# Kernel tuning notes

Measured on AMD Instinct MI355X. Metric: run time of the kernel, lower is better.

Reference implementation:

```python
import jax, jax.numpy as jnp
import numpy as np

B, S, D, L = 128, 256, 256, 3          # graphs, nodes/graph (=max_set_size), feat dim, gnn layers
E = 524288                              # edges per graph-set (avg degree 16)
N = B * S                               # total nodes per side
TAU, N_SINK, EPS_GIN, BN_EPS = 0.1, 20, 1.0, 1e-5


def setup_inputs() -> dict:
    key = jax.random.key(0)
    ks = jax.random.split(key, 16)
    sc = 1.0 / np.sqrt(D)
    inp = {
        "features_1": jax.random.normal(ks[0], (N, D), jnp.float32),
        "features_2": jax.random.normal(ks[1], (N, D), jnp.float32),
        "edge_index_1": jax.random.randint(ks[2], (2, E), 0, N),
        "edge_index_2": jax.random.randint(ks[3], (2, E), 0, N),
        "u_noise": jax.random.uniform(ks[4], (B, S, S), jnp.float32),
        # stacked GIN MLP params (3 identical-shape layers)
        "gin_w1": jax.random.normal(ks[5], (L, D, D), jnp.float32) * sc,
        "gin_b1": jnp.zeros((L, D), jnp.float32),
        "gin_w2": jax.random.normal(ks[6], (L, D, D), jnp.float32) * sc,
        "gin_b2": jnp.zeros((L, D), jnp.float32),
        "gin_gamma": jnp.ones((L, D), jnp.float32),
        "gin_beta": jnp.zeros((L, D), jnp.float32),
        # fc_transform1/2 and bilinear W
        "fc1_w": jax.random.normal(ks[7], (D, D), jnp.float32) * sc,
        "fc1_b": jnp.zeros((D,), jnp.float32),
        "fc2_w": jax.random.normal(ks[8], (D, D), jnp.float32) * sc,
        "fc2_b": jnp.zeros((D,), jnp.float32),
        "W": jax.random.normal(ks[9], (D, D), jnp.float32) * sc,
    }
    return inp


def _forward(features_1, features_2, u_noise, gin_w1, gin_b1, gin_w2, gin_b2,
             gin_gamma, gin_beta, fc1_w, fc1_b, fc2_w, fc2_b, W,
             edge_index_1, edge_index_2):
    def gin_stack(x, ei):
        src, dst = ei[0], ei[1]
        for l in range(L):
            # GINConv: nn((1+eps)*x + sum_{j->i} x_j), eps=True -> 1.0
            aggr = jax.ops.segment_sum(x[src], dst, num_segments=N)
            h = (1.0 + EPS_GIN) * x + aggr
            h = jax.nn.relu(h @ gin_w1[l] + gin_b1[l])
            h = h @ gin_w2[l] + gin_b2[l]
            mu = jnp.mean(h, axis=0)
            var = jnp.var(h, axis=0)                      # BatchNorm1d, training stats
            h = gin_gamma[l] * (h - mu) * jax.lax.rsqrt(var + BN_EPS) + gin_beta[l]
            x = jax.nn.relu(h)                            # outer relu (dropout p=0)
        return x

    g1 = gin_stack(features_1, edge_index_1).reshape(B, S, D)  # all graphs have S nodes -> no pad
    g2 = gin_stack(features_2, edge_index_2).reshape(B, S, D)

    def transform(g):
        return jax.nn.relu(g @ fc1_w + fc1_b) @ fc2_w + fc2_b

    m1 = transform(g1)   # masks are all-ones since every graph is full-size
    m2 = transform(g2)
    scores = jnp.einsum('bsd,de,bte->bst', m1, W, m2)          # [B,S,S]

    gumbel = -jnp.log(-jnp.log(u_noise + 1e-20) + 1e-20)
    log_alpha = (scores + gumbel) / TAU
    for _ in range(N_SINK):
        log_alpha = log_alpha - jax.scipy.special.logsumexp(log_alpha, axis=-1, keepdims=True)
        log_alpha = log_alpha - jax.scipy.special.logsumexp(log_alpha, axis=-2, keepdims=True)
    P = jnp.exp(log_alpha)

    p = jnp.sum(g1 - jnp.matmul(P, g2), axis=(1, 2))           # [B]
    p = (p - p.min()) / (p.max() - p.min())
    return jnp.exp(-p)


def reference(features_1, features_2, edge_index_1, edge_index_2, u_noise,
              gin_w1, gin_b1, gin_w2, gin_b2, gin_gamma, gin_beta,
              fc1_w, fc1_b, fc2_w, fc2_b, W):
    return _forward(features_1, features_2, u_noise, gin_w1, gin_b1, gin_w2, gin_b2,
                    gin_gamma, gin_beta, fc1_w, fc1_b, fc2_w, fc2_b, W,
                    edge_index_1, edge_index_2)
```

## Files before the change

kernel.cpp:

```cpp
#include <hip/hip_runtime.h>


constexpr int NNODE = 32768;
constexpr int NEDGE = 524288;

typedef __attribute__((ext_vector_type(8))) short bf16x8;
typedef __attribute__((ext_vector_type(4))) float f32x4;

__device__ __forceinline__ float bf2f(unsigned short u) {
  return __uint_as_float((unsigned)u << 16);
}
__device__ __forceinline__ unsigned short f2bf(float f) {
  unsigned u = __float_as_uint(f);
  return (unsigned short)((u + 0x7FFFu + ((u >> 16) & 1u)) >> 16);
}
__device__ __forceinline__ unsigned packbf(float a, float b) {
  return (unsigned)f2bf(a) | ((unsigned)f2bf(b) << 16);
}

__global__ __launch_bounds__(256) void k_conv(const float* __restrict__ a,
                                              const float* __restrict__ b,
                                              unsigned short* __restrict__ out) {
  size_t i = (size_t)blockIdx.x * 256 + threadIdx.x;
  const float* src = (i < 2097152) ? (a + i * 4) : (b + (i - 2097152) * 4);
  float4 v = *(const float4*)src;
  ushort4 o;
  o.x = f2bf(v.x); o.y = f2bf(v.y); o.z = f2bf(v.z); o.w = f2bf(v.w);
  *(ushort4*)(out + i * 4) = o;
}

__global__ __launch_bounds__(256) void k_wprep(const float* __restrict__ gw1,
                                               const float* __restrict__ gw2,
                                               unsigned short* __restrict__ Wt) {
  __shared__ float sh[64][65];
  int b = blockIdx.x;
  int mat = b >> 4, tile = b & 15;
  int tr = (tile >> 2) * 64, tc = (tile & 3) * 64;
  const float* src = (mat < 3) ? (gw1 + (size_t)mat * 65536) : (gw2 + (size_t)(mat - 3) * 65536);
  int t = threadIdx.x;
#pragma unroll
  for (int i = 0; i < 4; i++) {
    int c = t + i * 256;
    int row = c >> 4, c4 = (c & 15) * 4;
    float4 v = *(const float4*)(src + (size_t)(tr + row) * 256 + tc + c4);
    sh[row][c4] = v.x; sh[row][c4 + 1] = v.y; sh[row][c4 + 2] = v.z; sh[row][c4 + 3] = v.w;
  }
  __syncthreads();
#pragma unroll
  for (int i = 0; i < 2; i++) {
    int c = t + i * 256;
    int n = c >> 3, kc = (c & 7) * 8;
    unsigned short e[8];
#pragma unroll
    for (int j = 0; j < 8; j++) e[j] = f2bf(sh[kc + j][n]);
    uint4 o;
    o.x = e[0] | ((unsigned)e[1] << 16);
    o.y = e[2] | ((unsigned)e[3] << 16);
    o.z = e[4] | ((unsigned)e[5] << 16);
    o.w = e[6] | ((unsigned)e[7] << 16);
    *(uint4*)(Wt + (size_t)mat * 65536 + (size_t)(tc + n) * 256 + tr + kc) = o;
  }
}

__global__ void k_degree2(const int* __restrict__ e1, const int* __restrict__ e2,
                          int* __restrict__ cnt) {
  int b = blockIdx.x;
  int side = b >> 11;
  int e = (b & 2047) * 256 + threadIdx.x;
  const int* dst = (side ? e2 : e1) + NEDGE;
  atomicAdd(&cnt[side * NNODE + dst[e]], 1);
}

__global__ void k_scan2(const int* __restrict__ cnt, int* __restrict__ off,
                        int* __restrict__ cur) {
  __shared__ int sh[1024];
  int side = blockIdx.x;
  const int* c = cnt + side * NNODE;
  int* of = off + side * (NNODE + 64);
  int* cu = cur + side * NNODE;
  int t = threadIdx.x;
  int base = t * 32;
  int loc[32];
  int s = 0;
#pragma unroll
  for (int j = 0; j < 32; j++) { loc[j] = c[base + j]; s += loc[j]; }
  sh[t] = s;
  __syncthreads();
  for (int d = 1; d < 1024; d <<= 1) {
    int v = (t >= d) ? sh[t - d] : 0;
    __syncthreads();
    sh[t] += v;
    __syncthreads();
  }
  int run = sh[t] - s;
#pragma unroll
  for (int j = 0; j < 32; j++) { of[base + j] = run; cu[base + j] = run; run += loc[j]; }
  if (t == 1023) of[NNODE] = run;
}

__global__ void k_scatter2(const int* __restrict__ e1, const int* __restrict__ e2,
                           int* __restrict__ cur, int* __restrict__ srcs) {
  int b = blockIdx.x;
  int side = b >> 11;
  int e = (b & 2047) * 256 + threadIdx.x;
  const int* ei = (side ? e2 : e1);
  int d = ei[NEDGE + e];
  int p = atomicAdd(&cur[side * NNODE + d], 1);
  srcs[side * NEDGE + p] = ei[e];
}

template <bool BN>
__global__ __launch_bounds__(512, 4) void k_layer(
    const unsigned short* __restrict__ x,
    const int* __restrict__ off, const int* __restrict__ srcs,
    const float* __restrict__ pstats,
    const float* __restrict__ pgamma, const float* __restrict__ pbeta,
    const unsigned short* __restrict__ w1t,
    const unsigned short* __restrict__ w2t,
    const float* __restrict__ b1, const float* __restrict__ b2,
    float* __restrict__ stats,
    unsigned short* __restrict__ hout) {
  __shared__ __align__(16) char smem[69632];
  char* sA = smem;
  char* sA2 = smem;
  char* sW = smem + 32768;
  float2* red = (float2*)(smem + 65536);
  int tid = threadIdx.x;
  int lane = tid & 63, wid = tid >> 6;
  int wm = wid & 1, wn = wid >> 1;
  int q = lane >> 4, r = lane & 15;
  const int sw = (r & 7) << 4;
  int b = blockIdx.x;
  int side = b >> 9;
  size_t grow0 = (size_t)side * NNODE + (size_t)(b & 511) * 64;

  {
    int hw = tid >> 5, sub = tid & 31;
    float sc[8], shf[8];
    if (BN) {
      int c0 = sub * 8;
      const float* cs = pstats + side * 512;
      const float invn = 1.f / 32768.f;
#pragma unroll
      for (int j = 0; j < 8; j++) {
        float mu = cs[c0 + j] * invn;
        float var = cs[256 + c0 + j] * invn - mu * mu;
        float s = pgamma[c0 + j] * rsqrtf(var + 1e-5f);
        sc[j] = s; shf[j] = pbeta[c0 + j] - mu * s;
      }
    }
    const uint4* X = (const uint4*)x;
    size_t rbase = (size_t)side * NNODE;
    const int* offs = off + side * (NNODE + 64);
    const int* sr = srcs + (size_t)side * NEDGE;
#pragma unroll 1
    for (int nn = 0; nn < 4; nn++) {
      int lrow = hw * 4 + nn;
      int n = (int)(b & 511) * 64 + lrow;
      float a[8];
#pragma unroll
      for (int j = 0; j < 8; j++) a[j] = 0.f;
      auto acc8 = [&](uint4 u, float w) {
        unsigned uu[4] = {u.x, u.y, u.z, u.w};
#pragma unroll
        for (int j = 0; j < 4; j++) {
          float lo = __uint_as_float(uu[j] << 16);
          float hi = __uint_as_float(uu[j] & 0xFFFF0000u);
          if (BN) {
            lo = fmaxf(fmaf(lo, sc[2 * j], shf[2 * j]), 0.f);
            hi = fmaxf(fmaf(hi, sc[2 * j + 1], shf[2 * j + 1]), 0.f);
          }
          a[2 * j] = fmaf(lo, w, a[2 * j]);
          a[2 * j + 1] = fmaf(hi, w, a[2 * j + 1]);
        }
      };
      acc8(X[(rbase + n) * 32 + sub], 2.f);
      int e = offs[n], ee = offs[n + 1];
      for (; e + 3 < ee; e += 4) {
        int i0 = sr[e], i1 = sr[e + 1], i2 = sr[e + 2], i3 = sr[e + 3];
        uint4 u0 = X[(rbase + i0) * 32 + sub];
        uint4 u1 = X[(rbase + i1) * 32 + sub];
        uint4 u2 = X[(rbase + i2) * 32 + sub];
        uint4 u3 = X[(rbase + i3) * 32 + sub];
        acc8(u0, 1.f); acc8(u1, 1.f); acc8(u2, 1.f); acc8(u3, 1.f);
      }
      for (; e < ee; e++) acc8(X[(rbase + sr[e]) * 32 + sub], 1.f);
      uint4 o;
      o.x = packbf(a[0], a[1]); o.y = packbf(a[2], a[3]);
      o.z = packbf(a[4], a[5]); o.w = packbf(a[6], a[7]);
      *(uint4*)(sA + lrow * 512 + ((sub * 16) ^ ((lrow & 7) << 4))) = o;
    }
  }

  auto stageW = [&](const unsigned short* wsrc, int k0) {
    for (int c = tid; c < 2048; c += 512) {
      int row = c >> 3, cb = (c & 7) * 16;
      float4 v = *(const float4*)(wsrc + (size_t)row * 256 + k0 + (c & 7) * 8);
      *(float4*)(sW + row * 128 + (cb ^ ((row & 7) << 4))) = v;
    }
  };

  f32x4 acc[2][4];
#pragma unroll
  for (int mi = 0; mi < 2; mi++)
#pragma unroll
    for (int ni = 0; ni < 4; ni++) acc[mi][ni] = (f32x4){0.f, 0.f, 0.f, 0.f};

  stageW(w1t, 0);
  __syncthreads();

  for (int k0 = 0; k0 < 256; k0 += 64) {
#pragma unroll
    for (int ks = 0; ks < 2; ks++) {
      bf16x8 af[2], bfr[4];
      int cbA = (k0 * 2 + ks * 64 + q * 16) ^ sw;
      int cbW = (ks * 64 + q * 16) ^ sw;
#pragma unroll
      for (int mi = 0; mi < 2; mi++)
        af[mi] = *(const bf16x8*)(sA + (wm * 32 + mi * 16 + r) * 512 + cbA);
#pragma unroll
      for (int ni = 0; ni < 4; ni++)
        bfr[ni] = *(const bf16x8*)(sW + (wn * 64 + ni * 16 + r) * 128 + cbW);
#pragma unroll
      for (int mi = 0; mi < 2; mi++)
#pragma unroll
        for (int ni = 0; ni < 4; ni++)
          acc[mi][ni] = __builtin_amdgcn_mfma_f32_16x16x32_bf16(af[mi], bfr[ni], acc[mi][ni], 0, 0, 0);
    }
    __syncthreads();
    if (k0 < 192) {
      stageW(w1t, k0 + 64);
      __syncthreads();
    }
  }

  float b1v[4];
#pragma unroll
  for (int ni = 0; ni < 4; ni++) b1v[ni] = b1[wn * 64 + ni * 16 + r];
#pragma unroll
  for (int mi = 0; mi < 2; mi++)
#pragma unroll
    for (int ni = 0; ni < 4; ni++)
#pragma unroll
      for (int j = 0; j < 4; j++) {
        float o = fmaxf(acc[mi][ni][j] + b1v[ni], 0.f);
        int rowc = wm * 32 + mi * 16 + q * 4 + j;
        int colc = wn * 64 + ni * 16 + r;
        *(unsigned short*)(sA2 + rowc * 512 + ((colc * 2) ^ (((q * 4 + j) & 7) << 4))) = f2bf(o);
      }
#pragma unroll
  for (int mi = 0; mi < 2; mi++)
#pragma unroll
    for (int ni = 0; ni < 4; ni++) acc[mi][ni] = (f32x4){0.f, 0.f, 0.f, 0.f};
  stageW(w2t, 0);
  __syncthreads();

  for (int k0 = 0; k0 < 256; k0 += 64) {
#pragma unroll
    for (int ks = 0; ks < 2; ks++) {
      bf16x8 af[2], bfr[4];
      int cbA = (k0 * 2 + ks * 64 + q * 16) ^ sw;
      int cbW = (ks * 64 + q * 16) ^ sw;
#pragma unroll
      for (int mi = 0; mi < 2; mi++)
        af[mi] = *(const bf16x8*)(sA2 + (wm * 32 + mi * 16 + r) * 512 + cbA);
#pragma unroll
      for (int ni = 0; ni < 4; ni++)
        bfr[ni] = *(const bf16x8*)(sW + (wn * 64 + ni * 16 + r) * 128 + cbW);
#pragma unroll
      for (int mi = 0; mi < 2; mi++)
#pragma unroll
        for (int ni = 0; ni < 4; ni++)
          acc[mi][ni] = __builtin_amdgcn_mfma_f32_16x16x32_bf16(af[mi], bfr[ni], acc[mi][ni], 0, 0, 0);
    }
    __syncthreads();
    if (k0 < 192) {
      stageW(w2t, k0 + 64);
      __syncthreads();
    }
  }

  float b2v[4];
#pragma unroll
  for (int ni = 0; ni < 4; ni++) b2v[ni] = b2[wn * 64 + ni * 16 + r];
#pragma unroll
  for (int ni = 0; ni < 4; ni++) {
    float ss = 0.f, sq = 0.f;
#pragma unroll
    for (int mi = 0; mi < 2; mi++)
#pragma unroll
      for (int j = 0; j < 4; j++) {
        float o = acc[mi][ni][j] + b2v[ni];
        acc[mi][ni][j] = o;
        ss += o; sq += o * o;
      }
    ss += __shfl_xor(ss, 16, 64); ss += __shfl_xor(ss, 32, 64);
    sq += __shfl_xor(sq, 16, 64); sq += __shfl_xor(sq, 32, 64);
    if (q == 0) {
      float2 w; w.x = ss; w.y = sq;
      red[(wn * 64 + ni * 16 + r) * 2 + wm] = w;
    }
  }
#pragma unroll
  for (int mi = 0; mi < 2; mi++)
#pragma unroll
    for (int ni = 0; ni < 4; ni++)
#pragma unroll
      for (int j = 0; j < 4; j++) {
        int rowc = wm * 32 + mi * 16 + q * 4 + j;
        int colc = wn * 64 + ni * 16 + r;
        *(unsigned short*)(sW + rowc * 512 + ((colc * 2) ^ (((q * 4 + j) & 7) << 4))) =
            f2bf(acc[mi][ni][j]);
      }
  __syncthreads();
  float* cs = stats + side * 512;
  if (tid < 256) {
    float2 a = red[tid * 2], c2 = red[tid * 2 + 1];
    atomicAdd(&cs[tid], a.x + c2.x);
    atomicAdd(&cs[256 + tid], a.y + c2.y);
  }
  for (int c = tid; c < 2048; c += 512) {
    int row = c >> 5, cb = (c & 31) * 16;
    float4 v = *(const float4*)(sW + row * 512 + (cb ^ ((row & 7) << 4)));
    *(float4*)(hout + (grow0 + row) * 256 + (c & 31) * 8) = v;
  }
}

__global__ __launch_bounds__(256) void k_gsum(
    const unsigned short* __restrict__ h, const float* __restrict__ stats,
    const float* __restrict__ gamma, const float* __restrict__ beta,
    float* __restrict__ sg) {
  int b = blockIdx.x;
  int side = b >> 7, g = b & 127;
  int t = threadIdx.x;
  int c0 = (t & 63) * 4, rg = t >> 6;
  const float* cs = stats + side * 512;
  float sc[4], sh_[4];
#pragma unroll
  for (int j = 0; j < 4; j++) {
    float mu = cs[c0 + j] * (1.f / 32768.f);
    float var = cs[256 + c0 + j] * (1.f / 32768.f) - mu * mu;
    float s = gamma[c0 + j] * rsqrtf(var + 1e-5f);
    sc[j] = s; sh_[j] = beta[c0 + j] - mu * s;
  }
  size_t base = (size_t)side * NNODE + (size_t)g * 256;
  float acc = 0.f;
  for (int k = 0; k < 64; k++) {
    int row = rg + k * 4;
    ushort4 u = *(const ushort4*)(h + (base + row) * 256 + c0);
    acc += fmaxf(fmaf(bf2f(u.x), sc[0], sh_[0]), 0.f);
    acc += fmaxf(fmaf(bf2f(u.y), sc[1], sh_[1]), 0.f);
    acc += fmaxf(fmaf(bf2f(u.z), sc[2], sh_[2]), 0.f);
    acc += fmaxf(fmaf(bf2f(u.w), sc[3], sh_[3]), 0.f);
  }
  __shared__ float red[256];
  red[t] = acc;
  __syncthreads();
  if (t < 64) {
    float s = red[t] + red[t + 64] + red[t + 128] + red[t + 192];
#pragma unroll
    for (int m = 1; m < 64; m <<= 1) s += __shfl_xor(s, m, 64);
    if (t == 0) sg[b] = s;
  }
}

__global__ void k_final(const float* __restrict__ sg1, const float* __restrict__ sg2,
                        float* __restrict__ out) {
  int t = threadIdx.x;
  float a = sg1[t] - sg2[t];
  float b = sg1[t + 64] - sg2[t + 64];
  float mn = fminf(a, b), mx = fmaxf(a, b);
#pragma unroll
  for (int msk = 1; msk < 64; msk <<= 1) {
    mn = fminf(mn, __shfl_xor(mn, msk, 64));
    mx = fmaxf(mx, __shfl_xor(mx, msk, 64));
  }
  float inv = 1.0f / (mx - mn);
  out[t] = __expf(-(a - mn) * inv);
  out[t + 64] = __expf(-(b - mn) * inv);
}

extern "C" void kernel_launch(void* const* d_in, const int* in_sizes, int n_in,
                              void* d_out, int out_size, void* d_ws, size_t ws_size,
                              hipStream_t stream) {
  (void)in_sizes; (void)n_in; (void)out_size; (void)ws_size;
  const float* f1 = (const float*)d_in[0];
  const float* f2 = (const float*)d_in[1];
  const int* e1 = (const int*)d_in[2];
  const int* e2 = (const int*)d_in[3];
  const float* gw1 = (const float*)d_in[5];
  const float* gb1 = (const float*)d_in[6];
  const float* gw2 = (const float*)d_in[7];
  const float* gb2 = (const float*)d_in[8];
  const float* gga = (const float*)d_in[9];
  const float* gbe = (const float*)d_in[10];
  float* out = (float*)d_out;

  char* ws = (char*)d_ws;
  size_t o = 0;
  auto alloc = [&](size_t bytes) { void* p = ws + o; o += (bytes + 255) & ~(size_t)255; return p; };
  unsigned short* hb0 = (unsigned short*)alloc(2ull * NNODE * 256 * 2);
  unsigned short* hb1 = (unsigned short*)alloc(2ull * NNODE * 256 * 2);
  unsigned short* Wt = (unsigned short*)alloc(6ull * 65536 * 2);
  float* stats = (float*)alloc(3 * 1024 * 4);
  float* sg = (float*)alloc(256 * 4);
  int* cnt = (int*)alloc(2 * NNODE * 4);
  int* off = (int*)alloc(2 * (NNODE + 64) * 4);
  int* cur = (int*)alloc(2 * NNODE * 4);
  int* srcs = (int*)alloc(2ull * NEDGE * 4);

  (void)hipMemsetAsync(stats, 0, 3 * 1024 * 4, stream);
  (void)hipMemsetAsync(cnt, 0, 2 * NNODE * 4, stream);

  k_conv<<<16384, 256, 0, stream>>>(f1, f2, hb0);
  k_wprep<<<96, 256, 0, stream>>>(gw1, gw2, Wt);
  k_degree2<<<4096, 256, 0, stream>>>(e1, e2, cnt);
  k_scan2<<<2, 1024, 0, stream>>>(cnt, off, cur);
  k_scatter2<<<4096, 256, 0, stream>>>(e1, e2, cur, srcs);

  unsigned short* hb[2] = {hb0, hb1};
  for (int l = 0; l < 3; l++) {
    unsigned short* xin = hb[l & 1];
    unsigned short* hout = hb[1 - (l & 1)];
    if (l == 0)
      k_layer<false><<<1024, 512, 0, stream>>>(
          xin, off, srcs, nullptr, nullptr, nullptr,
          Wt + (size_t)l * 65536, Wt + (size_t)(3 + l) * 65536,
          gb1 + l * 256, gb2 + l * 256, stats + l * 1024, hout);
    else
      k_layer<true><<<1024, 512, 0, stream>>>(
          xin, off, srcs, stats + (l - 1) * 1024, gga + (l - 1) * 256, gbe + (l - 1) * 256,
          Wt + (size_t)l * 65536, Wt + (size_t)(3 + l) * 65536,
          gb1 + l * 256, gb2 + l * 256, stats + l * 1024, hout);
  }

  k_gsum<<<256, 256, 0, stream>>>(hb1, stats + 2 * 1024, gga + 512, gbe + 512, sg);
  k_final<<<1, 64, 0, stream>>>(sg, sg + 128, out);
}
```

Measured before the change: 501.4 us.

## Bucket CSR edges by source range to improve gather locality across blocks

Edges are split into four source-node buckets (by src>>13) within each destination's CSR segment, using per-bucket counts, offsets and cursors. The aggregation loop now walks bucket by bucket across a warp's four rows, so concurrent gathers across the GPU hit a narrower slice of the feature table at a time, which is meant to improve L2/cache hit rates. The W1 staging into shared memory is also moved ahead of aggregation so its global loads overlap with the gather. In exchange it adds an extra preprocessing kernel, larger count arrays, and keeps 32 accumulators per thread, which raises register pressure.

```diff
diff --git a/kernel.cpp b/kernel.cpp
--- a/kernel.cpp
+++ b/kernel.cpp
@@ -62,28 +62,31 @@
   }
 }
 
-__global__ void k_degree2(const int* __restrict__ e1, const int* __restrict__ e2,
-                          int* __restrict__ cnt) {
+__global__ void k_degree4(const int* __restrict__ e1, const int* __restrict__ e2,
+                          int* __restrict__ cnt4) {
   int b = blockIdx.x;
   int side = b >> 11;
   int e = (b & 2047) * 256 + threadIdx.x;
-  const int* dst = (side ? e2 : e1) + NEDGE;
-  atomicAdd(&cnt[side * NNODE + dst[e]], 1);
-}
-
-__global__ void k_scan2(const int* __restrict__ cnt, int* __restrict__ off,
-                        int* __restrict__ cur) {
+  const int* ei = (side ? e2 : e1);
+  int s = ei[e], d = ei[NEDGE + e];
+  atomicAdd(&cnt4[((size_t)side * NNODE + d) * 4 + (s >> 13)], 1);
+}
+
+__global__ void k_scan2(const int* __restrict__ cnt4, int* __restrict__ off) {
   __shared__ int sh[1024];
   int side = blockIdx.x;
-  const int* c = cnt + side * NNODE;
+  const int* c4 = cnt4 + (size_t)side * NNODE * 4;
   int* of = off + side * (NNODE + 64);
-  int* cu = cur + side * NNODE;
   int t = threadIdx.x;
   int base = t * 32;
   int loc[32];
   int s = 0;
 #pragma unroll
-  for (int j = 0; j < 32; j++) { loc[j] = c[base + j]; s += loc[j]; }
+  for (int j = 0; j < 32; j++) {
+    int n4 = (base + j) * 4;
+    loc[j] = c4[n4] + c4[n4 + 1] + c4[n4 + 2] + c4[n4 + 3];
+    s += loc[j];
+  }
   sh[t] = s;
   __syncthreads();
   for (int d = 1; d < 1024; d <<= 1) {
@@ -94,25 +97,41 @@
   }
   int run = sh[t] - s;
 #pragma unroll
-  for (int j = 0; j < 32; j++) { of[base + j] = run; cu[base + j] = run; run += loc[j]; }
+  for (int j = 0; j < 32; j++) { of[base + j] = run; run += loc[j]; }
   if (t == 1023) of[NNODE] = run;
 }
 
-__global__ void k_scatter2(const int* __restrict__ e1, const int* __restrict__ e2,
-                           int* __restrict__ cur, int* __restrict__ srcs) {
+__global__ __launch_bounds__(256) void k_suboff(const int* __restrict__ cnt4,
+                                                const int* __restrict__ off,
+                                                int* __restrict__ off2,
+                                                int* __restrict__ cur2) {
+  int i = blockIdx.x * 256 + threadIdx.x;
+  int side = i >> 15, n = i & 32767;
+  int base = off[side * (NNODE + 64) + n];
+  size_t i4 = (size_t)i * 4;
+  int c0 = cnt4[i4], c1 = cnt4[i4 + 1], c2 = cnt4[i4 + 2];
+  int o0 = base, o1 = base + c0, o2 = o1 + c1, o3 = o2 + c2;
+  off2[i4] = o0; off2[i4 + 1] = o1; off2[i4 + 2] = o2; off2[i4 + 3] = o3;
+  cur2[i4] = o0; cur2[i4 + 1] = o1; cur2[i4 + 2] = o2; cur2[i4 + 3] = o3;
+}
+
+__global__ void k_scatter4(const int* __restrict__ e1, const int* __restrict__ e2,
+                           int* __restrict__ cur2, int* __restrict__ srcs) {
   int b = blockIdx.x;
   int side = b >> 11;
   int e = (b & 2047) * 256 + threadIdx.x;
   const int* ei = (side ? e2 : e1);
-  int d = ei[NEDGE + e];
-  int p = atomicAdd(&cur[side * NNODE + d], 1);
-  srcs[side * NEDGE + p] = ei[e];
+  int s = ei[e], d = ei[NEDGE + e];
+  int p = atomicAdd(&cur2[((size_t)side * NNODE + d) * 4 + (s >> 13)], 1);
+  srcs[(size_t)side * NEDGE + p] = s;
 }
 
 template <bool BN>
 __global__ __launch_bounds__(512, 4) void k_layer(
     const unsigned short* __restrict__ x,
-    const int* __restrict__ off, const int* __restrict__ srcs,
+    const int* __restrict__ off,
+    const int* __restrict__ off2,
+    const int* __restrict__ srcs,
     const float* __restrict__ pstats,
     const float* __restrict__ pgamma, const float* __restrict__ pbeta,
     const unsigned short* __restrict__ w1t,
@@ -134,6 +153,16 @@
   int side = b >> 9;
   size_t grow0 = (size_t)side * NNODE + (size_t)(b & 511) * 64;
 
+  auto stageW = [&](const unsigned short* wsrc, int k0) {
+    for (int c = tid; c < 2048; c += 512) {
+      int row = c >> 3, cb = (c & 7) * 16;
+      float4 v = *(const float4*)(wsrc + (size_t)row * 256 + k0 + (c & 7) * 8);
+      *(float4*)(sW + row * 128 + (cb ^ ((row & 7) << 4))) = v;
+    }
+  };
+
+  stageW(w1t, 0);
+
   {
     int hw = tid >> 5, sub = tid & 31;
     float sc[8], shf[8];
@@ -152,61 +181,71 @@
     const uint4* X = (const uint4*)x;
     size_t rbase = (size_t)side * NNODE;
     const int* offs = off + side * (NNODE + 64);
+    const int* offs2 = off2 + (size_t)side * NNODE * 4;
     const int* sr = srcs + (size_t)side * NEDGE;
+    int nbase = (int)(b & 511) * 64 + hw * 4;
+
+    float a[4][8];
+#pragma unroll
+    for (int nn = 0; nn < 4; nn++)
+#pragma unroll
+      for (int j = 0; j < 8; j++) a[nn][j] = 0.f;
+
+    auto acc8 = [&](float* ap, uint4 u, float w) {
+      unsigned uu[4] = {u.x, u.y, u.z, u.w};
+#pragma unroll
+      for (int j = 0; j < 4; j++) {
+        float lo = __uint_as_float(uu[j] << 16);
+        float hi = __uint_as_float(uu[j] & 0xFFFF0000u);
+        if (BN) {
+          lo = fmaxf(fmaf(lo, sc[2 * j], shf[2 * j]), 0.f);
+          hi = fmaxf(fmaf(hi, sc[2 * j + 1], shf[2 * j + 1]), 0.f);
+        }
+        ap[2 * j] = fmaf(lo, w, ap[2 * j]);
+        ap[2 * j + 1] = fmaf(hi, w, ap[2 * j + 1]);
+      }
+    };
+
+#pragma unroll
+    for (int nn = 0; nn < 4; nn++)
+      acc8(a[nn], X[(rbase + nbase + nn) * 32 + sub], 2.f);
+
 #pragma unroll 1
+    for (int c = 0; c < 4; c++) {
+#pragma unroll
+      for (int nn = 0; nn < 4; nn++) {
+        int n = nbase + nn;
+        int e = offs2[(n << 2) + c];
+        int ee = (c < 3) ? offs2[(n << 2) + c + 1] : offs[n + 1];
+        for (; e + 3 < ee; e += 4) {
+          int i0 = sr[e], i1 = sr[e + 1], i2 = sr[e + 2], i3 = sr[e + 3];
+          uint4 u0 = X[(rbase + i0) * 32 + sub];
+          uint4 u1 = X[(rbase + i1) * 32 + sub];
+          uint4 u2 = X[(rbase + i2) * 32 + sub];
+          uint4 u3 = X[(rbase + i3) * 32 + sub];
+          acc8(a[nn], u0, 1.f); acc8(a[nn], u1, 1.f);
+          acc8(a[nn], u2, 1.f); acc8(a[nn], u3, 1.f);
+        }
+        for (; e < ee; e++) acc8(a[nn], X[(rbase + sr[e]) * 32 + sub], 1.f);
+      }
+    }
+
+#pragma unroll
     for (int nn = 0; nn < 4; nn++) {
       int lrow = hw * 4 + nn;
-      int n = (int)(b & 511) * 64 + lrow;
-      float a[8];
-#pragma unroll
-      for (int j = 0; j < 8; j++) a[j] = 0.f;
-      auto acc8 = [&](uint4 u, float w) {
-        unsigned uu[4] = {u.x, u.y, u.z, u.w};
-#pragma unroll
-        for (int j = 0; j < 4; j++) {
-          float lo = __uint_as_float(uu[j] << 16);
-          float hi = __uint_as_float(uu[j] & 0xFFFF0000u);
-          if (BN) {
-            lo = fmaxf(fmaf(lo, sc[2 * j], shf[2 * j]), 0.f);
-            hi = fmaxf(fmaf(hi, sc[2 * j + 1], shf[2 * j + 1]), 0.f);
-          }
-          a[2 * j] = fmaf(lo, w, a[2 * j]);
-          a[2 * j + 1] = fmaf(hi, w, a[2 * j + 1]);
-        }
-      };
-      acc8(X[(rbase + n) * 32 + sub], 2.f);
-      int e = offs[n], ee = offs[n + 1];
-      for (; e + 3 < ee; e += 4) {
-        int i0 = sr[e], i1 = sr[e + 1], i2 = sr[e + 2], i3 = sr[e + 3];
-        uint4 u0 = X[(rbase + i0) * 32 + sub];
-        uint4 u1 = X[(rbase + i1) * 32 + sub];
-        uint4 u2 = X[(rbase + i2) * 32 + sub];
-        uint4 u3 = X[(rbase + i3) * 32 + sub];
-        acc8(u0, 1.f); acc8(u1, 1.f); acc8(u2, 1.f); acc8(u3, 1.f);
-      }
-      for (; e < ee; e++) acc8(X[(rbase + sr[e]) * 32 + sub], 1.f);
       uint4 o;
-      o.x = packbf(a[0], a[1]); o.y = packbf(a[2], a[3]);
-      o.z = packbf(a[4], a[5]); o.w = packbf(a[6], a[7]);
+      o.x = packbf(a[nn][0], a[nn][1]); o.y = packbf(a[nn][2], a[nn][3]);
+      o.z = packbf(a[nn][4], a[nn][5]); o.w = packbf(a[nn][6], a[nn][7]);
       *(uint4*)(sA + lrow * 512 + ((sub * 16) ^ ((lrow & 7) << 4))) = o;
     }
   }
 
-  auto stageW = [&](const unsigned short* wsrc, int k0) {
-    for (int c = tid; c < 2048; c += 512) {
-      int row = c >> 3, cb = (c & 7) * 16;
-      float4 v = *(const float4*)(wsrc + (size_t)row * 256 + k0 + (c & 7) * 8);
-      *(float4*)(sW + row * 128 + (cb ^ ((row & 7) << 4))) = v;
-    }
-  };
-
   f32x4 acc[2][4];
 #pragma unroll
   for (int mi = 0; mi < 2; mi++)
 #pragma unroll
     for (int ni = 0; ni < 4; ni++) acc[mi][ni] = (f32x4){0.f, 0.f, 0.f, 0.f};
 
-  stageW(w1t, 0);
   __syncthreads();
 
   for (int k0 = 0; k0 < 256; k0 += 64) {
@@ -404,19 +443,21 @@
   unsigned short* Wt = (unsigned short*)alloc(6ull * 65536 * 2);
   float* stats = (float*)alloc(3 * 1024 * 4);
   float* sg = (float*)alloc(256 * 4);
-  int* cnt = (int*)alloc(2 * NNODE * 4);
+  int* cnt4 = (int*)alloc(2ull * NNODE * 4 * 4);
   int* off = (int*)alloc(2 * (NNODE + 64) * 4);
-  int* cur = (int*)alloc(2 * NNODE * 4);
+  int* off2 = (int*)alloc(2ull * NNODE * 4 * 4);
+  int* cur2 = (int*)alloc(2ull * NNODE * 4 * 4);
   int* srcs = (int*)alloc(2ull * NEDGE * 4);
 
   (void)hipMemsetAsync(stats, 0, 3 * 1024 * 4, stream);
-  (void)hipMemsetAsync(cnt, 0, 2 * NNODE * 4, stream);
+  (void)hipMemsetAsync(cnt4, 0, 2ull * NNODE * 4 * 4, stream);
 
   k_conv<<<16384, 256, 0, stream>>>(f1, f2, hb0);
   k_wprep<<<96, 256, 0, stream>>>(gw1, gw2, Wt);
-  k_degree2<<<4096, 256, 0, stream>>>(e1, e2, cnt);
-  k_scan2<<<2, 1024, 0, stream>>>(cnt, off, cur);
-  k_scatter2<<<4096, 256, 0, stream>>>(e1, e2, cur, srcs);
+  k_degree4<<<4096, 256, 0, stream>>>(e1, e2, cnt4);
+  k_scan2<<<2, 1024, 0, stream>>>(cnt4, off);
+  k_suboff<<<256, 256, 0, stream>>>(cnt4, off, off2, cur2);
+  k_scatter4<<<4096, 256, 0, stream>>>(e1, e2, cur2, srcs);
 
   unsigned short* hb[2] = {hb0, hb1};
   for (int l = 0; l < 3; l++) {
@@ -424,12 +465,12 @@
     unsigned short* hout = hb[1 - (l & 1)];
     if (l == 0)
       k_layer<false><<<1024, 512, 0, stream>>>(
-          xin, off, srcs, nullptr, nullptr, nullptr,
+          xin, off, off2, srcs, nullptr, nullptr, nullptr,
           Wt + (size_t)l * 65536, Wt + (size_t)(3 + l) * 65536,
           gb1 + l * 256, gb2 + l * 256, stats + l * 1024, hout);
     else
       k_layer<true><<<1024, 512, 0, stream>>>(
-          xin, off, srcs, stats + (l - 1) * 1024, gga + (l - 1) * 256, gbe + (l - 1) * 256,
+          xin, off, off2, srcs, stats + (l - 1) * 1024, gga + (l - 1) * 256, gbe + (l - 1) * 256,
           Wt + (size_t)l * 65536, Wt + (size_t)(3 + l) * 65536,
           gb1 + l * 256, gb2 + l * 256, stats + l * 1024, hout);
   }
```

Measured after the change: 572.1 us. 14.1% more time.

## Enlarge GIN layer row tile to 128 and fuse prep kernels

Applied to the files above, without the earlier changes.

The fused gather+MLP layer kernel now handles 128 rows per block instead of 64. Each warp computes a 64x64 output tile, and weights are staged in 32-wide K slices stored in a k-blocked layout with a new swizzle. This halves the number of blocks and the total weight re-staging per row. Separately, the conversion, weight-transpose and degree-count kernels are merged into one launch, and the prefix scan uses wave shuffles instead of a shared-memory Hillis-Steele loop. The larger LDS footprint (80KB) cuts resident blocks per CU, which may hurt latency hiding in the gather phase.

```diff
diff --git a/kernel.cpp b/kernel.cpp
--- a/kernel.cpp
+++ b/kernel.cpp
@@ -18,81 +18,94 @@
   return (unsigned)f2bf(a) | ((unsigned)f2bf(b) << 16);
 }
 
-__global__ __launch_bounds__(256) void k_conv(const float* __restrict__ a,
-                                              const float* __restrict__ b,
-                                              unsigned short* __restrict__ out) {
-  size_t i = (size_t)blockIdx.x * 256 + threadIdx.x;
-  const float* src = (i < 2097152) ? (a + i * 4) : (b + (i - 2097152) * 4);
-  float4 v = *(const float4*)src;
-  ushort4 o;
-  o.x = f2bf(v.x); o.y = f2bf(v.y); o.z = f2bf(v.z); o.w = f2bf(v.w);
-  *(ushort4*)(out + i * 4) = o;
-}
-
-__global__ __launch_bounds__(256) void k_wprep(const float* __restrict__ gw1,
-                                               const float* __restrict__ gw2,
-                                               unsigned short* __restrict__ Wt) {
+__global__ __launch_bounds__(256) void k_prep(
+    const float* __restrict__ f1, const float* __restrict__ f2,
+    unsigned short* __restrict__ hb0,
+    const float* __restrict__ gw1, const float* __restrict__ gw2,
+    unsigned short* __restrict__ Wt,
+    const int* __restrict__ e1, const int* __restrict__ e2,
+    int* __restrict__ cnt) {
   __shared__ float sh[64][65];
-  int b = blockIdx.x;
-  int mat = b >> 4, tile = b & 15;
-  int tr = (tile >> 2) * 64, tc = (tile & 3) * 64;
-  const float* src = (mat < 3) ? (gw1 + (size_t)mat * 65536) : (gw2 + (size_t)(mat - 3) * 65536);
-  int t = threadIdx.x;
-#pragma unroll
-  for (int i = 0; i < 4; i++) {
-    int c = t + i * 256;
-    int row = c >> 4, c4 = (c & 15) * 4;
-    float4 v = *(const float4*)(src + (size_t)(tr + row) * 256 + tc + c4);
-    sh[row][c4] = v.x; sh[row][c4 + 1] = v.y; sh[row][c4 + 2] = v.z; sh[row][c4 + 3] = v.w;
-  }
-  __syncthreads();
-#pragma unroll
-  for (int i = 0; i < 2; i++) {
-    int c = t + i * 256;
-    int n = c >> 3, kc = (c & 7) * 8;
-    unsigned short e[8];
-#pragma unroll
-    for (int j = 0; j < 8; j++) e[j] = f2bf(sh[kc + j][n]);
-    uint4 o;
-    o.x = e[0] | ((unsigned)e[1] << 16);
-    o.y = e[2] | ((unsigned)e[3] << 16);
-    o.z = e[4] | ((unsigned)e[5] << 16);
-    o.w = e[6] | ((unsigned)e[7] << 16);
-    *(uint4*)(Wt + (size_t)mat * 65536 + (size_t)(tc + n) * 256 + tr + kc) = o;
-  }
-}
-
-__global__ void k_degree2(const int* __restrict__ e1, const int* __restrict__ e2,
-                          int* __restrict__ cnt) {
-  int b = blockIdx.x;
-  int side = b >> 11;
-  int e = (b & 2047) * 256 + threadIdx.x;
-  const int* dst = (side ? e2 : e1) + NEDGE;
-  atomicAdd(&cnt[side * NNODE + dst[e]], 1);
-}
-
-__global__ void k_scan2(const int* __restrict__ cnt, int* __restrict__ off,
-                        int* __restrict__ cur) {
-  __shared__ int sh[1024];
+  int b = blockIdx.x, t = threadIdx.x;
+  if (b < 16384) {
+    size_t i = (size_t)b * 256 + t;
+    const float* src = (i < 2097152) ? (f1 + i * 4) : (f2 + (i - 2097152) * 4);
+    float4 v = *(const float4*)src;
+    ushort4 o;
+    o.x = f2bf(v.x); o.y = f2bf(v.y); o.z = f2bf(v.z); o.w = f2bf(v.w);
+    *(ushort4*)(hb0 + i * 4) = o;
+  } else if (b < 16480) {
+    int bb = b - 16384;
+    int mat = bb >> 4, tile = bb & 15;
+    int tr = (tile >> 2) * 64, tc = (tile & 3) * 64;
+    const float* src = (mat < 3) ? (gw1 + (size_t)mat * 65536) : (gw2 + (size_t)(mat - 3) * 65536);
+#pragma unroll
+    for (int i = 0; i < 4; i++) {
+      int c = t + i * 256;
+      int row = c >> 4, c4 = (c & 15) * 4;
+      float4 v = *(const float4*)(src + (size_t)(tr + row) * 256 + tc + c4);
+      sh[row][c4] = v.x; sh[row][c4 + 1] = v.y; sh[row][c4 + 2] = v.z; sh[row][c4 + 3] = v.w;
+    }
+    __syncthreads();
+#pragma unroll
+    for (int i = 0; i < 2; i++) {
+      int c = t + i * 256;
+      int n = c >> 3, kc = (c & 7) * 8;
+      unsigned short e[8];
+#pragma unroll
+      for (int j = 0; j < 8; j++) e[j] = f2bf(sh[kc + j][n]);
+      uint4 o;
+      o.x = e[0] | ((unsigned)e[1] << 16);
+      o.y = e[2] | ((unsigned)e[3] << 16);
+      o.z = e[4] | ((unsigned)e[5] << 16);
+      o.w = e[6] | ((unsigned)e[7] << 16);
+      int kg = tr + kc;
+      size_t idx = (size_t)mat * 65536 + (size_t)(kg >> 5) * 8192 + (size_t)(tc + n) * 32 + (kg & 31);
+      *(uint4*)(Wt + idx) = o;
+    }
+  } else {
+    int bb = b - 16480;
+    int side = bb >> 11;
+    int e = (bb & 2047) * 256 + t;
+    const int* dst = (side ? e2 : e1) + NEDGE;
+    atomicAdd(&cnt[side * NNODE + dst[e]], 1);
+  }
+}
+
+__global__ __launch_bounds__(1024) void k_scan2(const int* __restrict__ cnt,
+                                                int* __restrict__ off,
+                                                int* __restrict__ cur) {
   int side = blockIdx.x;
   const int* c = cnt + side * NNODE;
   int* of = off + side * (NNODE + 64);
   int* cu = cur + side * NNODE;
   int t = threadIdx.x;
+  int lane = t & 63, wv = t >> 6;
   int base = t * 32;
   int loc[32];
   int s = 0;
 #pragma unroll
   for (int j = 0; j < 32; j++) { loc[j] = c[base + j]; s += loc[j]; }
-  sh[t] = s;
-  __syncthreads();
-  for (int d = 1; d < 1024; d <<= 1) {
-    int v = (t >= d) ? sh[t - d] : 0;
-    __syncthreads();
-    sh[t] += v;
-    __syncthreads();
-  }
-  int run = sh[t] - s;
+  int tot = s;
+#pragma unroll
+  for (int d = 1; d < 64; d <<= 1) {
+    int v = __shfl_up(s, d, 64);
+    if (lane >= d) s += v;
+  }
+  __shared__ int ws[16];
+  if (lane == 63) ws[wv] = s;
+  __syncthreads();
+  if (t < 16) {
+    int w = ws[t];
+#pragma unroll
+    for (int d = 1; d < 16; d <<= 1) {
+      int v = __shfl_up(w, d, 64);
+      if (t >= d) w += v;
+    }
+    ws[t] = w;
+  }
+  __syncthreads();
+  int run = s - tot + (wv ? ws[wv - 1] : 0);
 #pragma unroll
   for (int j = 0; j < 32; j++) { of[base + j] = run; cu[base + j] = run; run += loc[j]; }
   if (t == 1023) of[NNODE] = run;
@@ -120,19 +133,33 @@
     const float* __restrict__ b1, const float* __restrict__ b2,
     float* __restrict__ stats,
     unsigned short* __restrict__ hout) {
-  __shared__ __align__(16) char smem[69632];
+  __shared__ __align__(16) char smem[81920];
   char* sA = smem;
   char* sA2 = smem;
-  char* sW = smem + 32768;
+  char* sW = smem + 65536;
   float2* red = (float2*)(smem + 65536);
   int tid = threadIdx.x;
   int lane = tid & 63, wid = tid >> 6;
   int wm = wid & 1, wn = wid >> 1;
   int q = lane >> 4, r = lane & 15;
-  const int sw = (r & 7) << 4;
+  const int swA = (r & 7) << 4;
+  const int swW = ((r >> 1) & 3) << 4;
   int b = blockIdx.x;
-  int side = b >> 9;
-  size_t grow0 = (size_t)side * NNODE + (size_t)(b & 511) * 64;
+  int side = b >> 8;
+  size_t grow0 = (size_t)side * NNODE + (size_t)(b & 255) * 128;
+
+  auto stageW = [&](const unsigned short* wsrc, int k0) {
+    const unsigned short* basep = wsrc + (size_t)(k0 >> 5) * 8192;
+#pragma unroll
+    for (int it = 0; it < 2; it++) {
+      int c = tid + it * 512;
+      int row = c >> 2, ch = c & 3;
+      float4 v = *(const float4*)(basep + (size_t)c * 8);
+      *(float4*)(sW + row * 64 + ((ch * 16) ^ (((row >> 1) & 3) << 4))) = v;
+    }
+  };
+
+  stageW(w1t, 0);
 
   {
     int hw = tid >> 5, sub = tid & 31;
@@ -153,10 +180,12 @@
     size_t rbase = (size_t)side * NNODE;
     const int* offs = off + side * (NNODE + 64);
     const int* sr = srcs + (size_t)side * NEDGE;
+    int nbase = (int)(b & 255) * 128;
+
 #pragma unroll 1
-    for (int nn = 0; nn < 4; nn++) {
-      int lrow = hw * 4 + nn;
-      int n = (int)(b & 511) * 64 + lrow;
+    for (int nn = 0; nn < 8; nn++) {
+      int lrow = hw * 8 + nn;
+      int n = nbase + lrow;
       float a[8];
 #pragma unroll
       for (int j = 0; j < 8; j++) a[j] = 0.f;
@@ -192,44 +221,32 @@
     }
   }
 
-  auto stageW = [&](const unsigned short* wsrc, int k0) {
-    for (int c = tid; c < 2048; c += 512) {
-      int row = c >> 3, cb = (c & 7) * 16;
-      float4 v = *(const float4*)(wsrc + (size_t)row * 256 + k0 + (c & 7) * 8);
-      *(float4*)(sW + row * 128 + (cb ^ ((row & 7) << 4))) = v;
-    }
-  };
-
-  f32x4 acc[2][4];
-#pragma unroll
-  for (int mi = 0; mi < 2; mi++)
+  f32x4 acc[4][4];
+#pragma unroll
+  for (int mi = 0; mi < 4; mi++)
 #pragma unroll
     for (int ni = 0; ni < 4; ni++) acc[mi][ni] = (f32x4){0.f, 0.f, 0.f, 0.f};
 
-  stageW(w1t, 0);
-  __syncthreads();
-
-  for (int k0 = 0; k0 < 256; k0 += 64) {
-#pragma unroll
-    for (int ks = 0; ks < 2; ks++) {
-      bf16x8 af[2], bfr[4];
-      int cbA = (k0 * 2 + ks * 64 + q * 16) ^ sw;
-      int cbW = (ks * 64 + q * 16) ^ sw;
-#pragma unroll
-      for (int mi = 0; mi < 2; mi++)
-        af[mi] = *(const bf16x8*)(sA + (wm * 32 + mi * 16 + r) * 512 + cbA);
+  __syncthreads();
+
+  for (int k0 = 0; k0 < 256; k0 += 32) {
+    bf16x8 af[4], bfr[4];
+    int cbA = (k0 * 2 + q * 16) ^ swA;
+    int cbW = (q * 16) ^ swW;
+#pragma unroll
+    for (int mi = 0; mi < 4; mi++)
+      af[mi] = *(const bf16x8*)(sA + (wm * 64 + mi * 16 + r) * 512 + cbA);
+#pragma unroll
+    for (int ni = 0; ni < 4; ni++)
+      bfr[ni] = *(const bf16x8*)(sW + (wn * 64 + ni * 16 + r) * 64 + cbW);
+#pragma unroll
+    for (int mi = 0; mi < 4; mi++)
 #pragma unroll
       for (int ni = 0; ni < 4; ni++)
-        bfr[ni] = *(const bf16x8*)(sW + (wn * 64 + ni * 16 + r) * 128 + cbW);
-#pragma unroll
-      for (int mi = 0; mi < 2; mi++)
-#pragma unroll
-        for (int ni = 0; ni < 4; ni++)
-          acc[mi][ni] = __builtin_amdgcn_mfma_f32_16x16x32_bf16(af[mi], bfr[ni], acc[mi][ni], 0, 0, 0);
-    }
+        acc[mi][ni] = __builtin_amdgcn_mfma_f32_16x16x32_bf16(af[mi], bfr[ni], acc[mi][ni], 0, 0, 0);
     __syncthreads();
-    if (k0 < 192) {
-      stageW(w1t, k0 + 64);
+    if (k0 < 224) {
+      stageW(w1t, k0 + 32);
       __syncthreads();
     }
   }
@@ -238,44 +255,41 @@
 #pragma unroll
   for (int ni = 0; ni < 4; ni++) b1v[ni] = b1[wn * 64 + ni * 16 + r];
 #pragma unroll
-  for (int mi = 0; mi < 2; mi++)
+  for (int mi = 0; mi < 4; mi++)
 #pragma unroll
     for (int ni = 0; ni < 4; ni++)
 #pragma unroll
       for (int j = 0; j < 4; j++) {
         float o = fmaxf(acc[mi][ni][j] + b1v[ni], 0.f);
-        int rowc = wm * 32 + mi * 16 + q * 4 + j;
+        int rowc = wm * 64 + mi * 16 + q * 4 + j;
         int colc = wn * 64 + ni * 16 + r;
         *(unsigned short*)(sA2 + rowc * 512 + ((colc * 2) ^ (((q * 4 + j) & 7) << 4))) = f2bf(o);
       }
 #pragma unroll
-  for (int mi = 0; mi < 2; mi++)
+  for (int mi = 0; mi < 4; mi++)
 #pragma unroll
     for (int ni = 0; ni < 4; ni++) acc[mi][ni] = (f32x4){0.f, 0.f, 0.f, 0.f};
   stageW(w2t, 0);
   __syncthreads();
 
-  for (int k0 = 0; k0 < 256; k0 += 64) {
-#pragma unroll
-    for (int ks = 0; ks < 2; ks++) {
-      bf16x8 af[2], bfr[4];
-      int cbA = (k0 * 2 + ks * 64 + q * 16) ^ sw;
-      int cbW = (ks * 64 + q * 16) ^ sw;
-#pragma unroll
-      for (int mi = 0; mi < 2; mi++)
-        af[mi] = *(const bf16x8*)(sA2 + (wm * 32 + mi * 16 + r) * 512 + cbA);
+  for (int k0 = 0; k0 < 256; k0 += 32) {
+    bf16x8 af[4], bfr[4];
+    int cbA = (k0 * 2 + q * 16) ^ swA;
+    int cbW = (q * 16) ^ swW;
+#pragma unroll
+    for (int mi = 0; mi < 4; mi++)
+      af[mi] = *(const bf16x8*)(sA2 + (wm * 64 + mi * 16 + r) * 512 + cbA);
+#pragma unroll
+    for (int ni = 0; ni < 4; ni++)
+      bfr[ni] = *(const bf16x8*)(sW + (wn * 64 + ni * 16 + r) * 64 + cbW);
+#pragma unroll
+    for (int mi = 0; mi < 4; mi++)
 #pragma unroll
       for (int ni = 0; ni < 4; ni++)
-        bfr[ni] = *(const bf16x8*)(sW + (wn * 64 + ni * 16 + r) * 128 + cbW);
-#pragma unroll
-      for (int mi = 0; mi < 2; mi++)
-#pragma unroll
-        for (int ni = 0; ni < 4; ni++)
-          acc[mi][ni] = __builtin_amdgcn_mfma_f32_16x16x32_bf16(af[mi], bfr[ni], acc[mi][ni], 0, 0, 0);
-    }
+        acc[mi][ni] = __builtin_amdgcn_mfma_f32_16x16x32_bf16(af[mi], bfr[ni], acc[mi][ni], 0, 0, 0);
     __syncthreads();
-    if (k0 < 192) {
-      stageW(w2t, k0 + 64);
+    if (k0 < 224) {
+      stageW(w2t, k0 + 32);
       __syncthreads();
     }
   }
@@ -287,7 +301,7 @@
   for (int ni = 0; ni < 4; ni++) {
     float ss = 0.f, sq = 0.f;
 #pragma unroll
-    for (int mi = 0; mi < 2; mi++)
+    for (int mi = 0; mi < 4; mi++)
 #pragma unroll
       for (int j = 0; j < 4; j++) {
         float o = acc[mi][ni][j] + b2v[ni];
@@ -302,14 +316,14 @@
     }
   }
 #pragma unroll
-  for (int mi = 0; mi < 2; mi++)
+  for (int mi = 0; mi < 4; mi++)
 #pragma unroll
     for (int ni = 0; ni < 4; ni++)
 #pragma unroll
       for (int j = 0; j < 4; j++) {
-        int rowc = wm * 32 + mi * 16 + q * 4 + j;
+        int rowc = wm * 64 + mi * 16 + q * 4 + j;
         int colc = wn * 64 + ni * 16 + r;
-        *(unsigned short*)(sW + rowc * 512 + ((colc * 2) ^ (((q * 4 + j) & 7) << 4))) =
+        *(unsigned short*)(sA2 + rowc * 512 + ((colc * 2) ^ (((q * 4 + j) & 7) << 4))) =
             f2bf(acc[mi][ni][j]);
       }
   __syncthreads();
@@ -319,9 +333,9 @@
     atomicAdd(&cs[tid], a.x + c2.x);
     atomicAdd(&cs[256 + tid], a.y + c2.y);
   }
-  for (int c = tid; c < 2048; c += 512) {
+  for (int c = tid; c < 4096; c += 512) {
     int row = c >> 5, cb = (c & 31) * 16;
-    float4 v = *(const float4*)(sW + row * 512 + (cb ^ ((row & 7) << 4)));
+    float4 v = *(const float4*)(sA2 + row * 512 + (cb ^ ((row & 7) << 4)));
     *(float4*)(hout + (grow0 + row) * 256 + (c & 31) * 8) = v;
   }
 }
@@ -412,9 +426,7 @@
   (void)hipMemsetAsync(stats, 0, 3 * 1024 * 4, stream);
   (void)hipMemsetAsync(cnt, 0, 2 * NNODE * 4, stream);
 
-  k_conv<<<16384, 256, 0, stream>>>(f1, f2, hb0);
-  k_wprep<<<96, 256, 0, stream>>>(gw1, gw2, Wt);
-  k_degree2<<<4096, 256, 0, stream>>>(e1, e2, cnt);
+  k_prep<<<20576, 256, 0, stream>>>(f1, f2, hb0, gw1, gw2, Wt, e1, e2, cnt);
   k_scan2<<<2, 1024, 0, stream>>>(cnt, off, cur);
   k_scatter2<<<4096, 256, 0, stream>>>(e1, e2, cur, srcs);
 
@@ -423,12 +435,12 @@
     unsigned short* xin = hb[l & 1];
     unsigned short* hout = hb[1 - (l & 1)];
     if (l == 0)
-      k_layer<false><<<1024, 512, 0, stream>>>(
+      k_layer<false><<<512, 512, 0, stream>>>(
           xin, off, srcs, nullptr, nullptr, nullptr,
           Wt + (size_t)l * 65536, Wt + (size_t)(3 + l) * 65536,
           gb1 + l * 256, gb2 + l * 256, stats + l * 1024, hout);
     else
-      k_layer<true><<<1024, 512, 0, stream>>>(
+      k_layer<true><<<512, 512, 0, stream>>>(
           xin, off, srcs, stats + (l - 1) * 1024, gga + (l - 1) * 256, gbe + (l - 1) * 256,
           Wt + (size_t)l * 65536, Wt + (size_t)(3 + l) * 65536,
           gb1 + l * 256, gb2 + l * 256, stats + l * 1024, hout);
```

After: 488.0 us. 2.7% less time.
